# Kernel optimization log

Measured on AMD Instinct MI355X. Metric: run time of the kernel, lower is better.

## Reference

```python
import jax, jax.numpy as jnp
import numpy as np

N, C, T, V = 64, 64, 128, 25
OUT, REL = 64, 8
MID = OUT // 2
BN_EPS = 1e-5


def _conv1x1(x, w, b):
    # 1x1 Conv2d: x [n,c,h,w_], w [o,c], b [o]
    return jnp.einsum('nchw,oc->nohw', x, w) + b[None, :, None, None]


def _forward(x, A, w1, b1, w2, b2, w11, b11, w22, b22, w3, b3, w4, b4,
             watt, batt, w5, b5, wc1, bc1, bn_g, bn_b, bn_m, bn_v,
             wc2, bc2, ws, bs, beita, alpha):
    T_ = x.shape[2]
    rel = w1.shape[0]
    x1 = _conv1x1(x, w1, b1)                          # [N,rel,T,V]
    x2 = _conv1x1(x, w2, b2)
    x1_mean, x2_mean = x1.mean(2), x2.mean(2)         # [N,rel,V]
    x1_max, x2_max = x1.max(2), x2.max(2)
    mean_res = x1_mean[:, :, :, None] - x2_mean[:, :, None, :]   # [N,rel,V,V]
    max_res = x1_max[:, :, :, None] - x2_max[:, :, None, :]
    # conv5: grouped 1x1 conv (groups=rel, 2 in-ch/group). The cat(dim=2)+reshape
    # interleaves channels as (mean[c], max[c]) pairs, so per-group it is:
    x_1 = jnp.tanh(w5[None, :, 0, None, None] * mean_res
                   + w5[None, :, 1, None, None] * max_res
                   + b5[None, :, None, None]) * alpha
    x_1 = _conv1x1(x_1, w4, b4)                       # [N,out,V,V]
    x3 = _conv1x1(x, w3, b3)                          # [N,out,T,V]
    x1_res = x_1 + A[None, None]
    # channel-wise spatial correlation attention
    att = jnp.tanh(jnp.einsum('nctu,nctv->ncuv', x1, x2) / T_)
    att = _conv1x1(att, watt, batt)                   # [N,out,V,V]
    global_res = jnp.einsum('nctu,ncuv->nctv', x3, att)
    # Bi_Inter 'channel': global avg pool -> 1x1 -> BN(inference) -> GELU -> 1x1 -> sigmoid
    g = global_res.mean((2, 3), keepdims=True)        # [N,out,1,1]
    h = _conv1x1(g, wc1, bc1)
    h = (h - bn_m[None, :, None, None]) * (bn_g[None, :, None, None]
        / jnp.sqrt(bn_v[None, :, None, None] + BN_EPS)) + bn_b[None, :, None, None]
    h = jax.nn.gelu(h, approximate=False)
    c_att = jax.nn.sigmoid(_conv1x1(h, wc2, bc2))     # [N,out,1,1]
    x1_res = c_att * x1_res
    x1_res = jnp.einsum('ncuv,nctv->nctu', x1_res, x3)  # [N,out,T,V]
    # Bi_Inter 'spatial': mean over T -> 1x1 (out->1) -> sigmoid
    s_att = jax.nn.sigmoid(_conv1x1(x1_res.mean(2, keepdims=True), ws, bs))  # [N,1,1,V]
    global_res = global_res * s_att
    x1_res = x1_res + global_res
    # per-frame spatial correlation (temporal branch)
    x11 = _conv1x1(x, w11, b11)
    x22 = _conv1x1(x, w22, b22)
    xt = jnp.tanh(jnp.einsum('nctv,nctu->ntvu', x11, x22) / rel)  # [N,T,V,V]
    t_res = jnp.einsum('nctu,ntuv->nctv', x3, xt)
    return t_res * beita + x1_res                     # [N,out,T,V]


def setup_inputs() -> dict:
    key = jax.random.key(0)
    ks = jax.random.split(key, 16)
    def nrm(i, shape, s=0.05):
        return jax.random.normal(ks[i], shape, jnp.float32) * s
    return {
        'x': jax.random.normal(ks[0], (N, C, T, V), jnp.float32),
        'A': nrm(1, (V, V), 0.1),
        'w1': nrm(2, (REL, C)), 'b1': jnp.zeros((REL,), jnp.float32),
        'w2': nrm(3, (REL, C)), 'b2': jnp.zeros((REL,), jnp.float32),
        'w11': nrm(4, (REL, C)), 'b11': jnp.zeros((REL,), jnp.float32),
        'w22': nrm(5, (REL, C)), 'b22': jnp.zeros((REL,), jnp.float32),
        'w3': nrm(6, (OUT, C)), 'b3': jnp.zeros((OUT,), jnp.float32),
        'w4': nrm(7, (OUT, REL)), 'b4': jnp.zeros((OUT,), jnp.float32),
        'watt': nrm(8, (OUT, REL)), 'batt': jnp.zeros((OUT,), jnp.float32),
        'w5': nrm(9, (REL, 2)), 'b5': jnp.zeros((REL,), jnp.float32),
        'wc1': nrm(10, (MID, OUT)), 'bc1': jnp.zeros((MID,), jnp.float32),
        'bn_g': jnp.ones((MID,), jnp.float32), 'bn_b': jnp.zeros((MID,), jnp.float32),
        'bn_m': jnp.zeros((MID,), jnp.float32), 'bn_v': jnp.ones((MID,), jnp.float32),
        'wc2': nrm(11, (OUT, MID)), 'bc2': jnp.zeros((OUT,), jnp.float32),
        'ws': nrm(12, (1, OUT)), 'bs': jnp.zeros((1,), jnp.float32),
        'beita': jnp.full((1,), 0.5, jnp.float32),
        'alpha': 1,
    }


def reference(x, A, w1, b1, w2, b2, w11, b11, w22, b22, w3, b3, w4, b4,
              watt, batt, w5, b5, wc1, bc1, bn_g, bn_b, bn_m, bn_v,
              wc2, bc2, ws, bs, beita, alpha):
    return _forward(x, A, w1, b1, w2, b2, w11, b11, w22, b22, w3, b3, w4, b4,
                    watt, batt, w5, b5, wc1, bc1, bn_g, bn_b, bn_m, bn_v,
                    wc2, bc2, ws, bs, beita, alpha)
```

## Files before the change

### kernel.cpp

```cpp
#include <hip/hip_runtime.h>
#include <hip/hip_bf16.h>
#include <math.h>

#define N_   64
#define C_   64
#define T_   128
#define V_   25
#define OUT_ 64
#define REL_ 8
#define MID_ 32
#define TV_  (T_*V_)
#define VV_  (V_*V_)
#define TT2  8
#define XTP3 40

typedef __hip_bfloat16 bf16;
typedef unsigned int uint;
typedef __attribute__((ext_vector_type(8))) short short8v;
typedef __attribute__((ext_vector_type(4))) float float4v;
__device__ __forceinline__ float b2f(bf16 x){ return __bfloat162float(x); }
__device__ __forceinline__ bf16  f2b(float x){ return __float2bfloat16(x); }
__device__ __forceinline__ float bfu(uint u){ return __uint_as_float(u<<16); }
__device__ __forceinline__ float bfh(uint u){ return __uint_as_float(u&0xffff0000u); }
__device__ __forceinline__ float bfs(unsigned short s){ return __uint_as_float(((uint)s)<<16); }

__device__ __forceinline__ float ftanh(float x){
    float cx = fminf(fmaxf(x, -15.f), 15.f);
    float e  = __expf(2.0f*cx);
    return (e - 1.0f) / (e + 1.0f);
}


__global__ __launch_bounds__(256) void k0_prep(
    const float* __restrict__ w1, const float* __restrict__ b1,
    const float* __restrict__ w2, const float* __restrict__ b2,
    const float* __restrict__ w11, const float* __restrict__ b11,
    const float* __restrict__ w22, const float* __restrict__ b22,
    const float* __restrict__ w3, const float* __restrict__ b3,
    unsigned short* __restrict__ WfragUS, float* __restrict__ Bg)
{
    int tid = threadIdx.x;
    for (int idx = tid; idx < 6144; idx += 256){
        int e  = idx & 7;
        int ln = (idx >> 3) & 63;
        int kb = (idx >> 9) & 1;
        int mt = idx >> 10;
        int m = mt*16 + (ln & 15);
        int k = kb*32 + ((ln >> 4) * 8) + e;
        float w;
        if      (m < 8)  w = w1[m*C_+k];
        else if (m < 16) w = w2[(m-8)*C_+k];
        else if (m < 24) w = w11[(m-16)*C_+k];
        else if (m < 32) w = w22[(m-24)*C_+k];
        else             w = w3[(m-32)*C_+k];
        bf16 h = f2b(w);
        WfragUS[idx] = *(unsigned short*)&h;
    }
    if (tid < 96){
        int o = tid; float bb;
        if      (o < 8)  bb = b1[o];
        else if (o < 16) bb = b2[o-8];
        else if (o < 24) bb = b11[o-16];
        else if (o < 32) bb = b22[o-24];
        else             bb = b3[o-32];
        Bg[o] = bb;
    }
}

__global__ __launch_bounds__(256) void k1_mfma(
    const float* __restrict__ x,
    const unsigned short* __restrict__ WfragUS, const float* __restrict__ Bg,
    float* __restrict__ x1f, float* __restrict__ x2f,
    float* __restrict__ x11f, float* __restrict__ x22f,
    bf16* __restrict__ x3h)
{
    __shared__ __align__(16) float xl[C_*64];
    __shared__ float Bl[96];
    int bid = blockIdx.x;
    int n = bid / 50, jt = bid % 50;
    int j0 = jt * 64;
    int tid = threadIdx.x;
    for (int e = tid; e < 1024; e += 256){
        int c = e >> 4, j4 = e & 15;
        ((float4*)xl)[e] = ((const float4*)(x + (size_t)(n*C_+c)*TV_ + j0))[j4];
    }
    if (tid < 96) Bl[tid] = Bg[tid];
    __syncthreads();

    int wave = tid >> 6, lane = tid & 63;
    int l15 = lane & 15, lg = lane >> 4;
    const short8v* wf = (const short8v*)WfragUS;
    short8v a[6][2];
    #pragma unroll
    for (int mt = 0; mt < 6; ++mt)
        #pragma unroll
        for (int kb = 0; kb < 2; ++kb)
            a[mt][kb] = wf[(mt*2 + kb)*64 + lane];
    int jw = wave*16 + l15;
    short8v b[2];
    #pragma unroll
    for (int kb = 0; kb < 2; ++kb){
        short8v bb;
        #pragma unroll
        for (int e = 0; e < 8; ++e){
            bf16 h = f2b(xl[(kb*32 + lg*8 + e)*64 + jw]);
            bb[e] = *(short*)&h;
        }
        b[kb] = bb;
    }
    float4v acc[6];
    #pragma unroll
    for (int mt = 0; mt < 6; ++mt) acc[mt] = (float4v){0.f,0.f,0.f,0.f};
    #pragma unroll
    for (int kb = 0; kb < 2; ++kb)
        #pragma unroll
        for (int mt = 0; mt < 6; ++mt)
            acc[mt] = __builtin_amdgcn_mfma_f32_16x16x32_bf16(a[mt][kb], b[kb], acc[mt], 0, 0, 0);

    int pos = j0 + jw;
    #pragma unroll
    for (int mt = 0; mt < 6; ++mt){
        #pragma unroll
        for (int reg = 0; reg < 4; ++reg){
            int o = mt*16 + lg*4 + reg;
            float val = acc[mt][reg] + Bl[o];
            if (o < 32){
                float* dst = (o < 8)  ? x1f  + ((size_t)(n*REL_ + o     ))*TV_
                           : (o < 16) ? x2f  + ((size_t)(n*REL_ + o - 8 ))*TV_
                           : (o < 24) ? x11f + ((size_t)(n*REL_ + o - 16))*TV_
                                      : x22f + ((size_t)(n*REL_ + o - 24))*TV_;
                dst[pos] = val;
            } else {
                x3h[((size_t)(n*OUT_ + o - 32))*TV_ + pos] = f2b(val);
            }
        }
    }
}

__global__ __launch_bounds__(256) void k_x3bar2(const bf16* __restrict__ x3h,
                                                float* __restrict__ x3bar)
{
    __shared__ __align__(16) float xf[TV_];
    __shared__ float red[V_*8];
    int bid = blockIdx.x;
    int tid = threadIdx.x;
    for (int e = tid; e < 400; e += 256){
        uint4 p = ((const uint4*)(x3h + (size_t)bid*TV_))[e];
        float* d = xf + e*8;
        d[0]=bfu(p.x); d[1]=bfh(p.x); d[2]=bfu(p.y); d[3]=bfh(p.y);
        d[4]=bfu(p.z); d[5]=bfh(p.z); d[6]=bfu(p.w); d[7]=bfh(p.w);
    }
    __syncthreads();
    if (tid < 200){
        int v = tid % V_, g = tid / V_;
        float s = 0.f;
        #pragma unroll
        for (int k=0;k<16;++k) s += xf[(g*16+k)*V_ + v];
        red[g*V_+v] = s;
    }
    __syncthreads();
    if (tid < V_){
        float s = 0.f;
        #pragma unroll
        for (int g=0; g<8; ++g) s += red[g*V_+tid];
        x3bar[(size_t)bid*V_+tid] = s * (1.0f/T_);
    }
}

__global__ __launch_bounds__(256) void k3_att8_xm(
    const float* __restrict__ x1f, const float* __restrict__ x2f,
    const float* __restrict__ w5, const float* __restrict__ b5,
    const int* __restrict__ alpha,
    float* __restrict__ att8, float* __restrict__ xm)
{
    __shared__ __align__(16) float l1[TV_], l2[TV_];
    __shared__ float mu1l[V_], mu2l[V_], m1l[V_], m2l[V_];
    int bid = blockIdx.x;
    int tid = threadIdx.x;
    int r = bid % REL_;
    for (int e = tid; e < 800; e += 256){
        ((float4*)l1)[e] = ((const float4*)(x1f + (size_t)bid*TV_))[e];
        ((float4*)l2)[e] = ((const float4*)(x2f + (size_t)bid*TV_))[e];
    }
    __syncthreads();
    if (tid < 50){
        int v = tid % V_;
        const float* L = (tid < V_) ? l1 : l2;
        float s=0.f, mm=-1e30f;
        for (int t=0;t<T_;++t){
            float a = L[t*V_+v];
            s += a; mm = fmaxf(mm, a);
        }
        if (tid < V_){ mu1l[v]=s*(1.0f/T_); m1l[v]=mm; }
        else         { mu2l[v]=s*(1.0f/T_); m2l[v]=mm; }
    }
    __syncthreads();
    float w50=w5[r*2+0], w51=w5[r*2+1], b5r=b5[r];
    float af = (float)alpha[0];
    for (int idx=tid; idx<VV_; idx+=256){
        int u = idx/V_, v = idx%V_;
        float s=0.f;
        for (int t=0;t<T_;++t) s = fmaf(l1[t*V_+u], l2[t*V_+v], s);
        att8[(size_t)bid*VV_+idx] = ftanh(s*(1.0f/T_));
        float mr = mu1l[u]-mu2l[v];
        float xr = m1l[u]-m2l[v];
        xm[(size_t)bid*VV_+idx] = ftanh(fmaf(w50,mr,fmaf(w51,xr,b5r))) * af;
    }
}

__global__ __launch_bounds__(256) void k6_chatt2(
    const float* __restrict__ att8, const float* __restrict__ x3bar,
    const float* __restrict__ watt, const float* __restrict__ batt,
    const float* __restrict__ wc1, const float* __restrict__ bc1,
    const float* __restrict__ bng, const float* __restrict__ bnb,
    const float* __restrict__ bnm, const float* __restrict__ bnv,
    const float* __restrict__ wc2, const float* __restrict__ bc2,
    float* __restrict__ catt)
{
    __shared__ float rs8[REL_*V_];
    __shared__ float gl[OUT_];
    __shared__ float hl[MID_];
    int n = blockIdx.x, tid = threadIdx.x;
    if (tid < REL_*V_){
        int r = tid / V_, u = tid % V_;
        const float* p = att8 + (size_t)(n*REL_+r)*VV_ + u*V_;
        float s = 0.f;
        #pragma unroll
        for (int v=0;v<V_;++v) s += p[v];
        rs8[tid] = s;
    }
    __syncthreads();
    if (tid < OUT_){
        int c = tid;
        const float* xb = x3bar + (size_t)(n*OUT_+c)*V_;
        float xbr[V_], sb = 0.f;
        #pragma unroll
        for (int u=0;u<V_;++u){ xbr[u]=xb[u]; sb += xbr[u]; }
        float s = 0.f;
        #pragma unroll
        for (int r=0;r<REL_;++r){
            float d = 0.f;
            #pragma unroll
            for (int u=0;u<V_;++u) d = fmaf(xbr[u], rs8[r*V_+u], d);
            s = fmaf(watt[c*REL_+r], d, s);
        }
        gl[c] = (s + (float)V_*batt[c]*sb) * (1.0f/(float)V_);
    }
    __syncthreads();
    if (tid < MID_){
        float h = bc1[tid];
        for (int c=0;c<OUT_;++c) h = fmaf(wc1[tid*OUT_+c], gl[c], h);
        h = (h - bnm[tid]) * bng[tid] * rsqrtf(bnv[tid] + 1e-5f) + bnb[tid];
        h = 0.5f*h*(1.0f+erff(h*0.70710678118654752f));
        hl[tid]=h;
    }
    __syncthreads();
    if (tid < OUT_){
        float s = bc2[tid];
        for (int m=0;m<MID_;++m) s = fmaf(wc2[tid*MID_+m], hl[m], s);
        catt[n*OUT_+tid] = 1.0f/(1.0f+expf(-s));
    }
}

__global__ __launch_bounds__(256) void k8_satt3(
    const float* __restrict__ xm, const float* __restrict__ A,
    const float* __restrict__ catt, const float* __restrict__ x3bar,
    const float* __restrict__ w4, const float* __restrict__ b4,
    const float* __restrict__ wsp, const float* __restrict__ bsp,
    float* __restrict__ satt)
{
    __shared__ __align__(16) float xml[REL_*VV_];
    __shared__ __align__(16) float xbl[OUT_*V_];
    __shared__ float Al[VV_];
    __shared__ float w4l[OUT_*REL_];
    __shared__ float scl[OUT_];
    __shared__ float Wl[REL_*V_];
    __shared__ float Yl[V_];
    __shared__ float red[OUT_];
    int n = blockIdx.x, tid = threadIdx.x;
    for (int e=tid; e<1250; e+=256)
        ((float4*)xml)[e] = ((const float4*)(xm + (size_t)n*REL_*VV_))[e];
    for (int e=tid; e<400; e+=256)
        ((float4*)xbl)[e] = ((const float4*)(x3bar + (size_t)n*OUT_*V_))[e];
    for (int e=tid; e<VV_; e+=256) Al[e] = A[e];
    for (int e=tid; e<OUT_*REL_; e+=256) w4l[e] = w4[e];
    if (tid < OUT_) scl[tid] = wsp[tid]*catt[n*OUT_+tid];
    __syncthreads();
    if (tid < REL_*V_){
        int r = tid/V_, v = tid%V_;
        float s = 0.f;
        for (int c=0;c<OUT_;++c) s = fmaf(scl[c]*w4l[c*REL_+r], xbl[c*V_+v], s);
        Wl[tid] = s;
    } else if (tid < REL_*V_ + V_){
        int v = tid - REL_*V_;
        float s = 0.f;
        for (int c=0;c<OUT_;++c) s = fmaf(scl[c], xbl[c*V_+v], s);
        Yl[v] = s;
    }
    __syncthreads();
    if (tid < OUT_){
        float s1 = 0.f;
        #pragma unroll
        for (int v=0;v<V_;++v) s1 += xbl[tid*V_+v];
        red[tid] = scl[tid]*b4[tid]*s1;
    }
    __syncthreads();
    if (tid < V_){
        int u = tid;
        float acc = 0.f;
        #pragma unroll
        for (int r=0;r<REL_;++r){
            const float* xr = xml + r*VV_ + u*V_;
            const float* wr = Wl + r*V_;
            #pragma unroll
            for (int v=0;v<V_;++v) acc = fmaf(xr[v], wr[v], acc);
        }
        #pragma unroll
        for (int v=0;v<V_;++v) acc = fmaf(Al[u*V_+v], Yl[v], acc);
        float beta = 0.f;
        for (int c=0;c<OUT_;++c) beta += red[c];
        satt[n*V_+u] = 1.0f/(1.0f+expf(-(bsp[0]+acc+beta)));
    }
}

__global__ __launch_bounds__(256) void k_comb3(
    const bf16* __restrict__ x3h,
    const float* __restrict__ att8, const float* __restrict__ xm,
    const float* __restrict__ A,
    const float* __restrict__ watt, const float* __restrict__ batt,
    const float* __restrict__ w4, const float* __restrict__ b4,
    const float* __restrict__ catt, const float* __restrict__ satt,
    bf16* __restrict__ combh)
{
    __shared__ __align__(16) unsigned short x3s[TV_];
    __shared__ float Ml[VV_];
    __shared__ float sl[V_];
    __shared__ __align__(16) unsigned short cst[TV_];
    int bid = blockIdx.x;
    int n = bid >> 6, c = bid & 63;
    int tid = threadIdx.x;
    for (int e = tid; e < 400; e += 256)
        ((uint4*)x3s)[e] = ((const uint4*)(x3h + (size_t)bid*TV_))[e];
    if (tid < V_) sl[tid] = satt[n*V_+tid];
    float ca = catt[bid];
    float w4r[REL_], war[REL_];
    #pragma unroll
    for (int r=0;r<REL_;++r){ w4r[r] = w4[c*REL_+r]; war[r] = watt[c*REL_+r]; }
    float b4c = b4[c], bac = batt[c];
    const float* xmn = xm  + (size_t)n*REL_*VV_;
    const float* a8n = att8 + (size_t)n*REL_*VV_;
    __syncthreads();
    for (int e = tid; e < VV_; e += 256){
        int w = e/V_, u = e%V_;
        float xv = b4c, av = bac;
        #pragma unroll
        for (int r=0;r<REL_;++r){
            xv = fmaf(w4r[r], xmn[r*VV_ + e], xv);
            av = fmaf(war[r], a8n[r*VV_ + u*V_ + w], av);
        }
        Ml[e] = ca*(xv + A[e]) + av*sl[w];
    }
    __syncthreads();
    int vh = tid & 1, tq = tid >> 1;
    int v0 = vh*13, nv = vh ? 12 : 13;
    float x3r[V_];
    #pragma unroll
    for (int u=0;u<V_;++u) x3r[u] = bfs(x3s[tq*V_+u]);
    for (int i=0;i<nv;++i){
        int v = v0+i;
        float s=0.f;
        #pragma unroll
        for (int u=0;u<V_;++u) s = fmaf(Ml[v*V_+u], x3r[u], s);
        bf16 h = f2b(s);
        cst[tq*V_+v] = *(unsigned short*)&h;
    }
    __syncthreads();
    for (int e = tid; e < 400; e += 256)
        ((uint4*)(combh + (size_t)bid*TV_))[e] = ((const uint4*)cst)[e];
}

__global__ __launch_bounds__(512) void k10_final7(
    const float* __restrict__ x11f, const float* __restrict__ x22f,
    const bf16* __restrict__ x3h, const bf16* __restrict__ combh,
    const float* __restrict__ beita, float* __restrict__ out)
{
    __shared__ __align__(16) char stg[25600];
    __shared__ __align__(16) unsigned short xtl[TT2*V_*XTP3];
    int bid = blockIdx.x;
    int n = bid >> 4, tt = bid & 15;
    int t0 = tt * TT2;
    int tid = threadIdx.x;
    float* l11 = (float*)stg;
    float* l22 = (float*)(stg + 6400);
    for (int e = tid; e < 400; e += 512){
        int r = e / 50, rem = e % 50;
        ((float4*)l11)[e] = ((const float4*)(x11f + (size_t)(n*REL_+r)*TV_ + t0*V_))[rem];
        ((float4*)l22)[e] = ((const float4*)(x22f + (size_t)(n*REL_+r)*TV_ + t0*V_))[rem];
    }
    __syncthreads();
    for (int e = tid; e < TT2*VV_; e += 512){
        int ti = e / VV_, uv = e % VV_;
        int u = uv / V_, v = uv % V_;
        float s = 0.f;
        #pragma unroll
        for (int r = 0; r < REL_; ++r)
            s = fmaf(l11[r*200 + ti*V_ + u], l22[r*200 + ti*V_ + v], s);
        bf16 h = f2b(ftanh(s * 0.125f));
        xtl[ti*(V_*XTP3) + u*XTP3 + v] = *(unsigned short*)&h;
    }
    float bt = beita[0];
    int vh = tid >> 8;
    int c_local = (tid >> 3) & 31;
    int ti = tid & 7;
    for (int cr = 0; cr < 2; ++cr){
        int c0 = cr*32;
        __syncthreads();
        for (int e = tid; e < 1600; e += 512){
            int cl = e / 50, w = e % 50;
            size_t base = (size_t)(n*OUT_ + c0 + cl)*TV_ + (size_t)t0*V_;
            uint4 p = (w < 25) ? ((const uint4*)(combh + base))[w]
                               : ((const uint4*)(x3h  + base))[w-25];
            *(uint4*)(stg + cl*800 + (w<25 ? w*16 : 400 + (w-25)*16)) = p;
        }
        __syncthreads();
        const unsigned short* x3row = (const unsigned short*)(stg + c_local*800 + 400) + ti*V_;
        float acc[13];
        #pragma unroll
        for (int j=0;j<13;++j) acc[j]=0.f;
        int base_s = ti*(V_*XTP3) + vh*12;
        #pragma unroll
        for (int u=0;u<V_;++u){
            float xa = bfs(x3row[u]);
            const uint* xr = (const uint*)(xtl + base_s + u*XTP3);
            uint R[7];
            #pragma unroll
            for (int k=0;k<7;++k) R[k] = xr[k];
            if (vh == 0){
                #pragma unroll
                for (int k=0;k<6;++k){
                    acc[2*k]   = fmaf(xa, bfu(R[k]), acc[2*k]);
                    acc[2*k+1] = fmaf(xa, bfh(R[k]), acc[2*k+1]);
                }
                acc[12] = fmaf(xa, bfu(R[6]), acc[12]);
            } else {
                acc[0] = fmaf(xa, bfh(R[0]), acc[0]);
                #pragma unroll
                for (int k=1;k<6;++k){
                    acc[2*k-1] = fmaf(xa, bfu(R[k]), acc[2*k-1]);
                    acc[2*k]   = fmaf(xa, bfh(R[k]), acc[2*k]);
                }
                acc[11] = fmaf(xa, bfu(R[6]), acc[11]);
            }
        }
        const unsigned short* cmbrow =
            (const unsigned short*)(stg + c_local*800) + ti*V_ + vh*13;
        if (vh == 0){
            #pragma unroll
            for (int j=0;j<13;++j) acc[j] = fmaf(bt, acc[j], bfs(cmbrow[j]));
        } else {
            #pragma unroll
            for (int j=0;j<12;++j) acc[j] = fmaf(bt, acc[j], bfs(cmbrow[j]));
        }
        __syncthreads();
        float* orow = (float*)(stg + c_local*800 + ti*100) + vh*13;
        if (vh == 0){
            #pragma unroll
            for (int j=0;j<13;++j) orow[j] = acc[j];
        } else {
            #pragma unroll
            for (int j=0;j<12;++j) orow[j] = acc[j];
        }
        __syncthreads();
        for (int e = tid; e < 1600; e += 512){
            int cl = e / 50, q = e % 50;
            *(float4*)(out + (size_t)(n*OUT_ + c0 + cl)*TV_ + (size_t)t0*V_ + q*4) =
                *(const float4*)(stg + cl*800 + q*16);
        }
    }
}

extern "C" void kernel_launch(void* const* d_in, const int* in_sizes, int n_in,
                              void* d_out, int out_size, void* d_ws, size_t ws_size,
                              hipStream_t stream)
{
    const float* x    = (const float*)d_in[0];
    const float* A    = (const float*)d_in[1];
    const float* w1   = (const float*)d_in[2];  const float* b1  = (const float*)d_in[3];
    const float* w2   = (const float*)d_in[4];  const float* b2  = (const float*)d_in[5];
    const float* w11  = (const float*)d_in[6];  const float* b11 = (const float*)d_in[7];
    const float* w22  = (const float*)d_in[8];  const float* b22 = (const float*)d_in[9];
    const float* w3   = (const float*)d_in[10]; const float* b3  = (const float*)d_in[11];
    const float* w4   = (const float*)d_in[12]; const float* b4  = (const float*)d_in[13];
    const float* watt = (const float*)d_in[14]; const float* batt= (const float*)d_in[15];
    const float* w5   = (const float*)d_in[16]; const float* b5  = (const float*)d_in[17];
    const float* wc1  = (const float*)d_in[18]; const float* bc1 = (const float*)d_in[19];
    const float* bng  = (const float*)d_in[20]; const float* bnb = (const float*)d_in[21];
    const float* bnm  = (const float*)d_in[22]; const float* bnv = (const float*)d_in[23];
    const float* wc2  = (const float*)d_in[24]; const float* bc2 = (const float*)d_in[25];
    const float* wsp  = (const float*)d_in[26]; const float* bsp = (const float*)d_in[27];
    const float* beita= (const float*)d_in[28];
    const int*  alpha = (const int*)d_in[29];
    float* out = (float*)d_out;

    char* wsb = (char*)d_ws;
    size_t off = 0;
    auto alloc = [&](size_t bytes)->char*{
        char* p = wsb + off;
        off += (bytes + 255) & ~(size_t)255;
        return p;
    };
    float* x1f   = (float*)alloc((size_t)N_*REL_*TV_*4);
    float* x2f   = (float*)alloc((size_t)N_*REL_*TV_*4);
    float* x11f  = (float*)alloc((size_t)N_*REL_*TV_*4);
    float* x22f  = (float*)alloc((size_t)N_*REL_*TV_*4);
    bf16*  x3h   = (bf16*) alloc((size_t)N_*OUT_*TV_*2);
    bf16*  combh = (bf16*) alloc((size_t)N_*OUT_*TV_*2);
    float* att8  = (float*)alloc((size_t)N_*REL_*VV_*4);
    float* xm    = (float*)alloc((size_t)N_*REL_*VV_*4);
    float* x3bar = (float*)alloc((size_t)N_*OUT_*V_*4);
    float* catt  = (float*)alloc((size_t)N_*OUT_*4);
    float* satt  = (float*)alloc((size_t)N_*V_*4);
    unsigned short* WfragUS = (unsigned short*)alloc((size_t)6144*2);
    float* Bg    = (float*)alloc((size_t)96*4);
    (void)ws_size; (void)n_in; (void)in_sizes; (void)out_size;

    k0_prep<<<1, 256, 0, stream>>>(w1,b1, w2,b2, w11,b11, w22,b22, w3,b3, WfragUS, Bg);
    k1_mfma<<<N_*50, 256, 0, stream>>>(x, WfragUS, Bg, x1f, x2f, x11f, x22f, x3h);
    k_x3bar2<<<N_*OUT_, 256, 0, stream>>>(x3h, x3bar);
    k3_att8_xm<<<N_*REL_, 256, 0, stream>>>(x1f, x2f, w5, b5, alpha, att8, xm);
    k6_chatt2<<<N_, 256, 0, stream>>>(att8, x3bar, watt, batt,
                                      wc1, bc1, bng, bnb, bnm, bnv, wc2, bc2, catt);
    k8_satt3<<<N_, 256, 0, stream>>>(xm, A, catt, x3bar, w4, b4, wsp, bsp, satt);
    k_comb3<<<N_*OUT_, 256, 0, stream>>>(x3h, att8, xm, A, watt, batt, w4, b4,
                                         catt, satt, combh);
    k10_final7<<<N_*16, 512, 0, stream>>>(x11f, x22f, x3h, combh, beita, out);
}
```

Measured before the change: 141.6 us.

## Store x1/x2/x11/x22 as bf16 and compute channel correlation with MFMA

The four relation-channel intermediates are now written by the first projection kernel as bf16 instead of fp32, halving their global write and read traffic in the later kernels. The per-block 25x25 correlation over T, previously done with scalar FMA loops in LDS, now uses 16x16x32 bf16 MFMA tiles, with four waves covering a padded 32x32 output. The final kernel unpacks the bf16 x11/x22 tiles to fp32 in shared memory. Precision of these intermediates drops to bf16, which also affects the mean/max statistics.

```diff
diff --git a/kernel.cpp b/kernel.cpp
--- a/kernel.cpp
+++ b/kernel.cpp
@@ -70,8 +70,8 @@
 __global__ __launch_bounds__(256) void k1_mfma(
     const float* __restrict__ x,
     const unsigned short* __restrict__ WfragUS, const float* __restrict__ Bg,
-    float* __restrict__ x1f, float* __restrict__ x2f,
-    float* __restrict__ x11f, float* __restrict__ x22f,
+    bf16* __restrict__ x1h, bf16* __restrict__ x2h,
+    bf16* __restrict__ x11h, bf16* __restrict__ x22h,
     bf16* __restrict__ x3h)
 {
     __shared__ __align__(16) float xl[C_*64];
@@ -124,15 +124,12 @@
         for (int reg = 0; reg < 4; ++reg){
             int o = mt*16 + lg*4 + reg;
             float val = acc[mt][reg] + Bl[o];
-            if (o < 32){
-                float* dst = (o < 8)  ? x1f  + ((size_t)(n*REL_ + o     ))*TV_
-                           : (o < 16) ? x2f  + ((size_t)(n*REL_ + o - 8 ))*TV_
-                           : (o < 24) ? x11f + ((size_t)(n*REL_ + o - 16))*TV_
-                                      : x22f + ((size_t)(n*REL_ + o - 24))*TV_;
-                dst[pos] = val;
-            } else {
-                x3h[((size_t)(n*OUT_ + o - 32))*TV_ + pos] = f2b(val);
-            }
+            bf16* dst = (o < 8)  ? x1h  + ((size_t)(n*REL_ + o     ))*TV_
+                      : (o < 16) ? x2h  + ((size_t)(n*REL_ + o - 8 ))*TV_
+                      : (o < 24) ? x11h + ((size_t)(n*REL_ + o - 16))*TV_
+                      : (o < 32) ? x22h + ((size_t)(n*REL_ + o - 24))*TV_
+                                 : x3h  + ((size_t)(n*OUT_ + o - 32))*TV_;
+            dst[pos] = f2b(val);
         }
     }
 }
@@ -167,41 +164,61 @@
     }
 }
 
-__global__ __launch_bounds__(256) void k3_att8_xm(
-    const float* __restrict__ x1f, const float* __restrict__ x2f,
+__global__ __launch_bounds__(256) void k3_mfma(
+    const bf16* __restrict__ x1h, const bf16* __restrict__ x2h,
     const float* __restrict__ w5, const float* __restrict__ b5,
     const int* __restrict__ alpha,
     float* __restrict__ att8, float* __restrict__ xm)
 {
-    __shared__ __align__(16) float l1[TV_], l2[TV_];
+    __shared__ __align__(16) unsigned short l1[TV_], l2[TV_];
     __shared__ float mu1l[V_], mu2l[V_], m1l[V_], m2l[V_];
     int bid = blockIdx.x;
     int tid = threadIdx.x;
     int r = bid % REL_;
-    for (int e = tid; e < 800; e += 256){
-        ((float4*)l1)[e] = ((const float4*)(x1f + (size_t)bid*TV_))[e];
-        ((float4*)l2)[e] = ((const float4*)(x2f + (size_t)bid*TV_))[e];
+    for (int e = tid; e < 400; e += 256){
+        ((uint4*)l1)[e] = ((const uint4*)(x1h + (size_t)bid*TV_))[e];
+        ((uint4*)l2)[e] = ((const uint4*)(x2h + (size_t)bid*TV_))[e];
     }
     __syncthreads();
     if (tid < 50){
         int v = tid % V_;
-        const float* L = (tid < V_) ? l1 : l2;
+        const unsigned short* L = (tid < V_) ? l1 : l2;
         float s=0.f, mm=-1e30f;
         for (int t=0;t<T_;++t){
-            float a = L[t*V_+v];
+            float a = bfs(L[t*V_+v]);
             s += a; mm = fmaxf(mm, a);
         }
         if (tid < V_){ mu1l[v]=s*(1.0f/T_); m1l[v]=mm; }
         else         { mu2l[v]=s*(1.0f/T_); m2l[v]=mm; }
     }
     __syncthreads();
+    int wave = tid >> 6, lane = tid & 63;
+    int l15 = lane & 15, lg = lane >> 4;
+    int mt = wave >> 1, nt = wave & 1;
+    int mu = mt*16 + l15;
+    int nv = nt*16 + l15;
+    float4v acc = (float4v){0.f,0.f,0.f,0.f};
+    #pragma unroll
+    for (int kb = 0; kb < 4; ++kb){
+        short8v av, bv;
+        #pragma unroll
+        for (int e = 0; e < 8; ++e){
+            int k = kb*32 + lg*8 + e;
+            av[e] = (mu < V_) ? (short)l1[k*V_ + mu] : (short)0;
+            bv[e] = (nv < V_) ? (short)l2[k*V_ + nv] : (short)0;
+        }
+        acc = __builtin_amdgcn_mfma_f32_16x16x32_bf16(av, bv, acc, 0, 0, 0);
+    }
+    #pragma unroll
+    for (int reg = 0; reg < 4; ++reg){
+        int u = mt*16 + lg*4 + reg;
+        if (u < V_ && nv < V_)
+            att8[(size_t)bid*VV_ + u*V_ + nv] = ftanh(acc[reg]*(1.0f/T_));
+    }
     float w50=w5[r*2+0], w51=w5[r*2+1], b5r=b5[r];
     float af = (float)alpha[0];
     for (int idx=tid; idx<VV_; idx+=256){
         int u = idx/V_, v = idx%V_;
-        float s=0.f;
-        for (int t=0;t<T_;++t) s = fmaf(l1[t*V_+u], l2[t*V_+v], s);
-        att8[(size_t)bid*VV_+idx] = ftanh(s*(1.0f/T_));
         float mr = mu1l[u]-mu2l[v];
         float xr = m1l[u]-m2l[v];
         xm[(size_t)bid*VV_+idx] = ftanh(fmaf(w50,mr,fmaf(w51,xr,b5r))) * af;
@@ -380,7 +397,7 @@
 }
 
 __global__ __launch_bounds__(512) void k10_final7(
-    const float* __restrict__ x11f, const float* __restrict__ x22f,
+    const bf16* __restrict__ x11h, const bf16* __restrict__ x22h,
     const bf16* __restrict__ x3h, const bf16* __restrict__ combh,
     const float* __restrict__ beita, float* __restrict__ out)
 {
@@ -393,9 +410,14 @@
     float* l11 = (float*)stg;
     float* l22 = (float*)(stg + 6400);
     for (int e = tid; e < 400; e += 512){
-        int r = e / 50, rem = e % 50;
-        ((float4*)l11)[e] = ((const float4*)(x11f + (size_t)(n*REL_+r)*TV_ + t0*V_))[rem];
-        ((float4*)l22)[e] = ((const float4*)(x22f + (size_t)(n*REL_+r)*TV_ + t0*V_))[rem];
+        int half = (e >= 200);
+        int i = half ? e-200 : e;
+        int r = i / 25, ch = i % 25;
+        const bf16* src = (half ? x22h : x11h) + (size_t)(n*REL_+r)*TV_ + t0*V_ + ch*8;
+        uint4 p = *(const uint4*)src;
+        float* d = (half ? l22 : l11) + i*8;
+        d[0]=bfu(p.x); d[1]=bfh(p.x); d[2]=bfu(p.y); d[3]=bfh(p.y);
+        d[4]=bfu(p.z); d[5]=bfh(p.z); d[6]=bfu(p.w); d[7]=bfh(p.w);
     }
     __syncthreads();
     for (int e = tid; e < TT2*VV_; e += 512){
@@ -509,10 +531,10 @@
         off += (bytes + 255) & ~(size_t)255;
         return p;
     };
-    float* x1f   = (float*)alloc((size_t)N_*REL_*TV_*4);
-    float* x2f   = (float*)alloc((size_t)N_*REL_*TV_*4);
-    float* x11f  = (float*)alloc((size_t)N_*REL_*TV_*4);
-    float* x22f  = (float*)alloc((size_t)N_*REL_*TV_*4);
+    bf16*  x1h   = (bf16*) alloc((size_t)N_*REL_*TV_*2);
+    bf16*  x2h   = (bf16*) alloc((size_t)N_*REL_*TV_*2);
+    bf16*  x11h  = (bf16*) alloc((size_t)N_*REL_*TV_*2);
+    bf16*  x22h  = (bf16*) alloc((size_t)N_*REL_*TV_*2);
     bf16*  x3h   = (bf16*) alloc((size_t)N_*OUT_*TV_*2);
     bf16*  combh = (bf16*) alloc((size_t)N_*OUT_*TV_*2);
     float* att8  = (float*)alloc((size_t)N_*REL_*VV_*4);
@@ -525,13 +547,13 @@
     (void)ws_size; (void)n_in; (void)in_sizes; (void)out_size;
 
     k0_prep<<<1, 256, 0, stream>>>(w1,b1, w2,b2, w11,b11, w22,b22, w3,b3, WfragUS, Bg);
-    k1_mfma<<<N_*50, 256, 0, stream>>>(x, WfragUS, Bg, x1f, x2f, x11f, x22f, x3h);
+    k1_mfma<<<N_*50, 256, 0, stream>>>(x, WfragUS, Bg, x1h, x2h, x11h, x22h, x3h);
     k_x3bar2<<<N_*OUT_, 256, 0, stream>>>(x3h, x3bar);
-    k3_att8_xm<<<N_*REL_, 256, 0, stream>>>(x1f, x2f, w5, b5, alpha, att8, xm);
+    k3_mfma<<<N_*REL_, 256, 0, stream>>>(x1h, x2h, w5, b5, alpha, att8, xm);
     k6_chatt2<<<N_, 256, 0, stream>>>(att8, x3bar, watt, batt,
                                       wc1, bc1, bng, bnb, bnm, bnv, wc2, bc2, catt);
     k8_satt3<<<N_, 256, 0, stream>>>(xm, A, catt, x3bar, w4, b4, wsp, bsp, satt);
     k_comb3<<<N_*OUT_, 256, 0, stream>>>(x3h, att8, xm, A, watt, batt, w4, b4,
                                          catt, satt, combh);
-    k10_final7<<<N_*16, 512, 0, stream>>>(x11f, x22f, x3h, combh, beita, out);
-}
+    k10_final7<<<N_*16, 512, 0, stream>>>(x11h, x22h, x3h, combh, beita, out);
+}
```

Result: faster. 136.4 us (-3.6%).
